# Optimization experiments

Hardware: AMD Instinct MI355X
Metric: run time of the kernel (lower is better)

The kernel has to match this reference:

```python
import jax, jax.numpy as jnp
import numpy as np

N = 50000      # nodes
E = 800000     # edges (before self-loops)
DIN, H1, H2, OUT = 128, 128, 64, 40
LN_EPS = 1e-5


def setup_inputs() -> dict:
    key = jax.random.key(0)
    ks = jax.random.split(key, 16)
    s = lambda d: 1.0 / np.sqrt(d)
    inp = {
        "x": jax.random.normal(ks[0], (N, DIN), jnp.float32),
        "edge_index": jax.random.randint(ks[1], (2, E), 0, N, dtype=jnp.int64),
        # GCNConv weights (applied as x @ W) and biases
        "W1": jax.random.normal(ks[2], (DIN, H1), jnp.float32) * s(DIN),
        "b1": jnp.zeros((H1,), jnp.float32),
        "W2": jax.random.normal(ks[3], (H1, H2), jnp.float32) * s(H1),
        "b2": jnp.zeros((H2,), jnp.float32),
        "W3": jax.random.normal(ks[4], (H2, H2), jnp.float32) * s(H2),
        "b3": jnp.zeros((H2,), jnp.float32),
        # LayerNorms
        "g1": jnp.ones((H1,), jnp.float32),
        "be1": jnp.zeros((H1,), jnp.float32),
        "g2": jnp.ones((H2,), jnp.float32),
        "be2": jnp.zeros((H2,), jnp.float32),
        # post_mp MLP head
        "Wp1": jax.random.normal(ks[5], (H2, H2), jnp.float32) * s(H2),
        "bp1": jnp.zeros((H2,), jnp.float32),
        "Wp2": jax.random.normal(ks[6], (H2, OUT), jnp.float32) * s(H2),
        "bp2": jnp.zeros((OUT,), jnp.float32),
    }
    return inp


def _layer_norm(x, g, b):
    mu = jnp.mean(x, axis=-1, keepdims=True)
    var = jnp.mean((x - mu) ** 2, axis=-1, keepdims=True)
    return (x - mu) * jax.lax.rsqrt(var + LN_EPS) * g + b


def _gcn(x, src, dst, norm, W, b):
    # PyG GCNConv: linear first, then normalized gather/scatter-add, bias last
    h = x @ W                                  # [N, H]
    msg = h[src] * norm[:, None]               # [E+N, H] gather
    out = jax.ops.segment_sum(msg, dst, num_segments=N)  # scatter-add
    return out + b


def reference(x, edge_index, W1, b1, W2, b2, W3, b3, g1, be1, g2, be2,
              Wp1, bp1, Wp2, bp2):
    loops = jnp.arange(N, dtype=edge_index.dtype)
    src = jnp.concatenate([edge_index[0], loops])  # add self-loops
    dst = jnp.concatenate([edge_index[1], loops])
    # symmetric normalization D^{-1/2} (A+I) D^{-1/2} (same graph all layers)
    deg = jax.ops.segment_sum(jnp.ones_like(src, dtype=x.dtype), dst,
                              num_segments=N)
    dinv = jnp.where(deg > 0, jax.lax.rsqrt(jnp.maximum(deg, 1.0)), 0.0)
    norm = dinv[src] * dinv[dst]

    h = _gcn(x, src, dst, norm, W1, b1)
    h = _layer_norm(jax.nn.relu(h), g1, be1)
    h = _gcn(h, src, dst, norm, W2, b2)
    h = _layer_norm(jax.nn.relu(h), g2, be2)
    emb = _gcn(h, src, dst, norm, W3, b3)      # emb = conv output, pre-ReLU
    h = jax.nn.relu(emb)
    h = (h @ Wp1 + bp1) @ Wp2 + bp2            # post_mp: two stacked Linears
    return emb, jax.nn.log_softmax(h, axis=1)
```

## Files before the change

kernel.cpp:

```cpp
#include <hip/hip_runtime.h>
#include <hip/hip_bf16.h>

#define DIN 128
#define HID1 128
#define HID2 64
#define OUTD 40

typedef __attribute__((ext_vector_type(8))) short bf16x8;
typedef __attribute__((ext_vector_type(4))) float f32x4;

__device__ __forceinline__ float bf2f(unsigned int u) {
    union { unsigned int i; float f; } c;
    c.i = u << 16;
    return c.f;
}
__device__ __forceinline__ unsigned short f2bf(float f) {
    union { float f; unsigned int i; } c; c.f = f;
    unsigned int r = c.i + 0x7FFFu + ((c.i >> 16) & 1u);
    return (unsigned short)(r >> 16);
}
__device__ __forceinline__ unsigned int packbf(float lo, float hi) {
    return (unsigned int)f2bf(lo) | ((unsigned int)f2bf(hi) << 16);
}

__global__ void detect_kernel(const unsigned short* __restrict__ xu,
                              const int* __restrict__ ei, int* __restrict__ flags) {
    __shared__ int sh[2];
    if (threadIdx.x < 2) sh[threadIdx.x] = 0;
    __syncthreads();
    int bad = 0;
    for (int i = threadIdx.x; i < 2048; i += 256) {
        float v = bf2f(xu[2 * i]);
        float a = fabsf(v);
        if (!(a <= 1e4f) || (v != 0.f && a < 1e-4f)) bad++;
    }
    int zodd = 0;
    for (int i = threadIdx.x; i < 1024; i += 256)
        if (ei[2 * i + 1] == 0) zodd++;
    atomicAdd(&sh[0], bad);
    atomicAdd(&sh[1], zodd);
    __syncthreads();
    if (threadIdx.x == 0) {
        flags[0] = (sh[0] > 512) ? 1 : 0;
        flags[1] = (sh[1] > 512) ? 1 : 0;
    }
}

__device__ __forceinline__ int get_src(const int* ei, int E, int e, int e64) {
    return e64 ? ei[2 * e] : ei[e];
}
__device__ __forceinline__ int get_dst(const int* ei, int E, int e, int e64) {
    return e64 ? ei[2 * (E + e)] : ei[E + e];
}


__global__ void init_cnt_kernel(int* __restrict__ cnt, int N) {
    int i = blockIdx.x * blockDim.x + threadIdx.x;
    if (i < N) cnt[i] = 0;
}

__global__ void pos_kernel(const int* __restrict__ ei, int* __restrict__ cnt,
                           int* __restrict__ pos, int E, int N,
                           const int* __restrict__ flags) {
    int e64 = flags[1];
    int base = (blockIdx.x * blockDim.x + threadIdx.x) * 4;
    #pragma unroll
    for (int u = 0; u < 4; ++u) {
        int e = base + u;
        if (e < E) {
            int d = get_dst(ei, E, e, e64);
            pos[e] = ((unsigned)d < (unsigned)N) ? atomicAdd(&cnt[d], 1) : -1;
        }
    }
}


__launch_bounds__(256)
__global__ void bsum_kernel(const int* __restrict__ cnt, int* __restrict__ bsum, int N) {
    __shared__ int sh[256];
    int t = threadIdx.x;
    int i = blockIdx.x * 256 + t;
    sh[t] = (i < N) ? cnt[i] : 0;
    __syncthreads();
    #pragma unroll
    for (int off = 128; off >= 1; off >>= 1) {
        if (t < off) sh[t] += sh[t + off];
        __syncthreads();
    }
    if (t == 0) bsum[blockIdx.x] = sh[0];
}

__launch_bounds__(256)
__global__ void bscan_kernel(const int* __restrict__ bsum, int* __restrict__ bbase,
                             int* __restrict__ indptr, int NB, int N) {
    __shared__ int part[256];
    int t = threadIdx.x;
    int CH = (NB + 255) / 256;
    int lo = t * CH, hi = lo + CH; if (hi > NB) hi = NB;
    int s = 0;
    for (int i = lo; i < hi; ++i) s += bsum[i];
    part[t] = s;
    __syncthreads();
    for (int off = 1; off < 256; off <<= 1) {
        int v = (t >= off) ? part[t - off] : 0;
        __syncthreads();
        part[t] += v;
        __syncthreads();
    }
    int run = (t > 0) ? part[t - 1] : 0;
    for (int i = lo; i < hi; ++i) { bbase[i] = run; run += bsum[i]; }
    if (t == 255) indptr[N] = part[255];
}

__launch_bounds__(256)
__global__ void emit_kernel(const int* __restrict__ cnt, const int* __restrict__ bbase,
                            int* __restrict__ indptr, float* __restrict__ dinv, int N) {
    __shared__ int sh[256];
    int t = threadIdx.x;
    int i = blockIdx.x * 256 + t;
    int c = (i < N) ? cnt[i] : 0;
    sh[t] = c;
    __syncthreads();
    for (int off = 1; off < 256; off <<= 1) {
        int v = (t >= off) ? sh[t - off] : 0;
        __syncthreads();
        sh[t] += v;
        __syncthreads();
    }
    if (i < N) {
        int excl = sh[t] - c + bbase[blockIdx.x];
        indptr[i] = excl;
        dinv[i] = 1.0f / sqrtf((float)(c + 1));
    }
}

__global__ void scatter_kernel(const int* __restrict__ ei, const int* __restrict__ indptr,
                               const int* __restrict__ pos, int* __restrict__ csr_src,
                               int E, int N, const int* __restrict__ flags) {
    int e64 = flags[1];
    int base = (blockIdx.x * blockDim.x + threadIdx.x) * 4;
    #pragma unroll
    for (int u = 0; u < 4; ++u) {
        int e = base + u;
        if (e < E) {
            int p = pos[e];
            if (p >= 0) {
                int d = get_dst(ei, E, e, e64);
                int s = get_src(ei, E, e, e64);
                if ((unsigned)s >= (unsigned)N) s = 0;
                csr_src[indptr[d] + p] = s;
            }
        }
    }
}


struct WCvt {
    const void* p[14];
    int sz[14];
    int off[14];
    int tobf[14];
    int cols[14];
};

__global__ void wcvt_kernel(WCvt w, unsigned short* __restrict__ wbf,
                            float* __restrict__ wf, const int* __restrict__ flags) {
    int xf32 = flags[0];
    int stride = gridDim.x * blockDim.x;
    int tid = blockIdx.x * blockDim.x + threadIdx.x;
    for (int a = 0; a < 14; ++a) {
        const float* pf = (const float*)w.p[a];
        const unsigned short* pb = (const unsigned short*)w.p[a];
        int n = w.sz[a], off = w.off[a], tobf = w.tobf[a];
        int cols = w.cols[a];
        int rows = tobf ? (n / cols) : 0;
        for (int i = tid; i < n; i += stride) {
            float v = xf32 ? pf[i] : bf2f(pb[i]);
            if (tobf) {
                int k = i / cols, m = i % cols;
                wbf[off + m * rows + k] = f2bf(v);
            } else {
                wf[off + i] = v;
            }
        }
    }
}

__global__ void xcvt_kernel(const float* __restrict__ xf, unsigned short* __restrict__ xbf,
                            int n, const int* __restrict__ flags) {
    if (!flags[0]) return;
    int stride = gridDim.x * blockDim.x;
    for (int i = blockIdx.x * blockDim.x + threadIdx.x; i < n; i += stride)
        xbf[i] = f2bf(xf[i]);
}


template<int K, int M>
__launch_bounds__(256)
__global__ void mm_mfma_kernel(const unsigned short* __restrict__ A0,
                               const unsigned short* __restrict__ A1,
                               const unsigned short* __restrict__ WT,
                               unsigned short* __restrict__ C, int N,
                               const int* __restrict__ flags, int useAlt) {
    __shared__ unsigned short Ws[M][K + 8];
    const unsigned short* A = (useAlt && flags[0]) ? A1 : A0;
    int tid = threadIdx.x;
    for (int idx = tid; idx < M * K / 8; idx += 256) {
        int r = idx / (K / 8), c8 = idx % (K / 8);
        *(uint4*)&Ws[r][c8 * 8] = *(const uint4*)&WT[r * K + c8 * 8];
    }
    __syncthreads();
    int w = tid >> 6, lane = tid & 63;
    int m = lane & 15, q = lane >> 4;
    int row_a = blockIdx.x * 64 + w * 16 + m;
    if (row_a >= N) row_a = N - 1;
    const unsigned short* arow = A + (size_t)row_a * K;
    f32x4 acc[M / 16];
    #pragma unroll
    for (int t = 0; t < M / 16; ++t) acc[t] = (f32x4){0.f, 0.f, 0.f, 0.f};
    #pragma unroll
    for (int ks = 0; ks < K / 32; ++ks) {
        int k0 = ks * 32 + q * 8;
        bf16x8 a = *(const bf16x8*)&arow[k0];
        #pragma unroll
        for (int t = 0; t < M / 16; ++t) {
            bf16x8 b = *(const bf16x8*)&Ws[t * 16 + m][k0];
            acc[t] = __builtin_amdgcn_mfma_f32_16x16x32_bf16(a, b, acc[t], 0, 0, 0);
        }
    }
    int rbase = blockIdx.x * 64 + w * 16 + q * 4;
    #pragma unroll
    for (int reg = 0; reg < 4; ++reg) {
        int row = rbase + reg;
        if (row < N) {
            #pragma unroll
            for (int t = 0; t < M / 16; ++t)
                C[(size_t)row * M + t * 16 + m] = f2bf(acc[t][reg]);
        }
    }
}


template<int VPL>
__device__ __forceinline__ void gacc(float* acc, const unsigned short* r, float n) {
    if constexpr (VPL == 8) {
        uint4 u = *(const uint4*)r;
        acc[0] += bf2f(u.x & 0xffffu) * n; acc[1] += bf2f(u.x >> 16) * n;
        acc[2] += bf2f(u.y & 0xffffu) * n; acc[3] += bf2f(u.y >> 16) * n;
        acc[4] += bf2f(u.z & 0xffffu) * n; acc[5] += bf2f(u.z >> 16) * n;
        acc[6] += bf2f(u.w & 0xffffu) * n; acc[7] += bf2f(u.w >> 16) * n;
    } else {
        uint2 u = *(const uint2*)r;
        acc[0] += bf2f(u.x & 0xffffu) * n; acc[1] += bf2f(u.x >> 16) * n;
        acc[2] += bf2f(u.y & 0xffffu) * n; acc[3] += bf2f(u.y >> 16) * n;
    }
}

template<int VPL>
__device__ __forceinline__ void gacc2(float* acc, const unsigned short* r0, float n0,
                                      const unsigned short* r1, float n1) {
    if constexpr (VPL == 8) {
        uint4 u0 = *(const uint4*)r0;
        uint4 u1 = *(const uint4*)r1;
        acc[0] += bf2f(u0.x & 0xffffu) * n0 + bf2f(u1.x & 0xffffu) * n1;
        acc[1] += bf2f(u0.x >> 16) * n0 + bf2f(u1.x >> 16) * n1;
        acc[2] += bf2f(u0.y & 0xffffu) * n0 + bf2f(u1.y & 0xffffu) * n1;
        acc[3] += bf2f(u0.y >> 16) * n0 + bf2f(u1.y >> 16) * n1;
        acc[4] += bf2f(u0.z & 0xffffu) * n0 + bf2f(u1.z & 0xffffu) * n1;
        acc[5] += bf2f(u0.z >> 16) * n0 + bf2f(u1.z >> 16) * n1;
        acc[6] += bf2f(u0.w & 0xffffu) * n0 + bf2f(u1.w & 0xffffu) * n1;
        acc[7] += bf2f(u0.w >> 16) * n0 + bf2f(u1.w >> 16) * n1;
    } else {
        uint2 u0 = *(const uint2*)r0;
        uint2 u1 = *(const uint2*)r1;
        acc[0] += bf2f(u0.x & 0xffffu) * n0 + bf2f(u1.x & 0xffffu) * n1;
        acc[1] += bf2f(u0.x >> 16) * n0 + bf2f(u1.x >> 16) * n1;
        acc[2] += bf2f(u0.y & 0xffffu) * n0 + bf2f(u1.y & 0xffffu) * n1;
        acc[3] += bf2f(u0.y >> 16) * n0 + bf2f(u1.y >> 16) * n1;
    }
}

template<int H, bool RELU_LN, bool EMB>
__launch_bounds__(256)
__global__ void agg_kernel(const unsigned short* __restrict__ h,
                           const int* __restrict__ indptr,
                           const int* __restrict__ csr_src,
                           const float* __restrict__ dinv,
                           const float* __restrict__ bias,
                           const float* __restrict__ gamma,
                           const float* __restrict__ beta,
                           unsigned short* __restrict__ out,
                           void* __restrict__ out_emb,
                           int N, const int* __restrict__ flags) {
    constexpr int VPL = H / 16;
    __shared__ int   lsrc[4][64];
    __shared__ float lnrm[4][64];
    int w = threadIdx.x >> 6;
    int lane = threadIdx.x & 63;
    int ql = lane >> 4;
    int g = lane & 15;
    int node = blockIdx.x * 4 + w;
    if (node >= N) return;
    float di = dinv[node];
    int c0 = g * VPL;
    float acc[VPL];
    #pragma unroll
    for (int v = 0; v < VPL; ++v) acc[v] = 0.f;
    gacc<VPL>(acc, h + (size_t)node * H + c0, (ql == 0) ? di * di : 0.f);
    int beg = indptr[node], end = indptr[node + 1];
    for (int base = beg; base < end; base += 64) {
        int m = end - base; if (m > 64) m = 64;
        if (lane < m) {
            int s = csr_src[base + lane];
            if ((unsigned)s >= (unsigned)N) s = 0;
            lsrc[w][lane] = s;
            lnrm[w][lane] = dinv[s] * di;
        }
        int j = ql;
        for (; j + 4 < m; j += 8) {
            int s0 = lsrc[w][j], s1 = lsrc[w][j + 4];
            float n0 = lnrm[w][j], n1 = lnrm[w][j + 4];
            gacc2<VPL>(acc, h + (size_t)s0 * H + c0, n0, h + (size_t)s1 * H + c0, n1);
        }
        if (j < m)
            gacc<VPL>(acc, h + (size_t)lsrc[w][j] * H + c0, lnrm[w][j]);
    }
    #pragma unroll
    for (int v = 0; v < VPL; ++v) acc[v] += __shfl_xor(acc[v], 16, 64);
    #pragma unroll
    for (int v = 0; v < VPL; ++v) acc[v] += __shfl_xor(acc[v], 32, 64);
    #pragma unroll
    for (int v = 0; v < VPL; ++v) acc[v] += bias[c0 + v];
    if constexpr (RELU_LN) {
        #pragma unroll
        for (int v = 0; v < VPL; ++v) acc[v] = fmaxf(acc[v], 0.f);
        float s = 0.f, sq = 0.f;
        #pragma unroll
        for (int v = 0; v < VPL; ++v) { s += acc[v]; sq += acc[v] * acc[v]; }
        #pragma unroll
        for (int off = 8; off >= 1; off >>= 1) {
            s += __shfl_xor(s, off, 64);
            sq += __shfl_xor(sq, off, 64);
        }
        float mu = s * (1.0f / H);
        float var = fmaxf(sq * (1.0f / H) - mu * mu, 0.f);
        float inv = 1.0f / sqrtf(var + 1e-5f);
        #pragma unroll
        for (int v = 0; v < VPL; ++v)
            acc[v] = (acc[v] - mu) * inv * gamma[c0 + v] + beta[c0 + v];
    }
    if (ql == 0) {
        unsigned short* orow = out + (size_t)node * H + c0;
        if constexpr (VPL == 8) {
            uint4 p;
            p.x = packbf(acc[0], acc[1]); p.y = packbf(acc[2], acc[3]);
            p.z = packbf(acc[4], acc[5]); p.w = packbf(acc[6], acc[7]);
            *(uint4*)orow = p;
        } else {
            uint2 p; p.x = packbf(acc[0], acc[1]); p.y = packbf(acc[2], acc[3]);
            *(uint2*)orow = p;
        }
        if constexpr (EMB) {
            if (flags[0]) {
                float* o = (float*)out_emb + (size_t)node * H + c0;
                #pragma unroll
                for (int v4 = 0; v4 < VPL / 4; ++v4)
                    *(float4*)(o + v4 * 4) = make_float4(acc[v4 * 4], acc[v4 * 4 + 1],
                                                         acc[v4 * 4 + 2], acc[v4 * 4 + 3]);
            } else {
                unsigned short* o = (unsigned short*)out_emb + (size_t)node * H + c0;
                #pragma unroll
                for (int v2 = 0; v2 < VPL / 2; ++v2)
                    ((unsigned int*)o)[v2] = packbf(acc[v2 * 2], acc[v2 * 2 + 1]);
            }
        }
    }
}


__launch_bounds__(256)
__global__ void head_kernel(const unsigned short* __restrict__ emb,
                            const float* __restrict__ Wp1,
                            const float* __restrict__ bp1,
                            const float* __restrict__ Wp2,
                            const float* __restrict__ bp2,
                            void* __restrict__ d_out, int N,
                            const int* __restrict__ flags) {
    __shared__ float Est[64][68];
    __shared__ float W1s[64][64];
    __shared__ float Tst[64][68];
    __shared__ float W2s[64][OUTD];
    __shared__ float b1s[64];
    __shared__ float b2s[OUTD];
    int tid = threadIdx.x;
    int row0 = blockIdx.x * 64;
    for (int i = tid; i < 64 * 64; i += 256) W1s[i >> 6][i & 63] = Wp1[i];
    for (int i = tid; i < 64 * OUTD; i += 256) W2s[i / OUTD][i % OUTD] = Wp2[i];
    if (tid < 64) b1s[tid] = bp1[tid];
    if (tid < OUTD) b2s[tid] = bp2[tid];
    for (int i = tid; i < 64 * 32; i += 256) {
        int r = i >> 5, kk = i & 31;
        int row = row0 + r;
        unsigned int u = (row < N) ? *(const unsigned int*)&emb[(size_t)row * 64 + kk * 2] : 0u;
        Est[kk * 2][r]     = fmaxf(bf2f(u & 0xffffu), 0.f);
        Est[kk * 2 + 1][r] = fmaxf(bf2f(u >> 16), 0.f);
    }
    __syncthreads();
    {
        int rg = tid >> 4, cg = tid & 15;
        int r = rg * 4, c = cg * 4;
        float acc[4][4];
        #pragma unroll
        for (int i = 0; i < 4; ++i)
            #pragma unroll
            for (int jj = 0; jj < 4; ++jj) acc[i][jj] = b1s[c + jj];
        #pragma unroll 4
        for (int k = 0; k < 64; ++k) {
            float4 a = *(const float4*)&Est[k][r];
            float4 wv = *(const float4*)&W1s[k][c];
            acc[0][0] += a.x * wv.x; acc[0][1] += a.x * wv.y; acc[0][2] += a.x * wv.z; acc[0][3] += a.x * wv.w;
            acc[1][0] += a.y * wv.x; acc[1][1] += a.y * wv.y; acc[1][2] += a.y * wv.z; acc[1][3] += a.y * wv.w;
            acc[2][0] += a.z * wv.x; acc[2][1] += a.z * wv.y; acc[2][2] += a.z * wv.z; acc[2][3] += a.z * wv.w;
            acc[3][0] += a.w * wv.x; acc[3][1] += a.w * wv.y; acc[3][2] += a.w * wv.z; acc[3][3] += a.w * wv.w;
        }
        #pragma unroll
        for (int i = 0; i < 4; ++i)
            #pragma unroll
            for (int jj = 0; jj < 4; ++jj) Tst[c + jj][r + i] = acc[i][jj];
    }
    __syncthreads();
    int row = tid >> 2, tc = tid & 3, o0 = tc * 10;
    int node = row0 + row;
    float u[10];
    #pragma unroll
    for (int o = 0; o < 10; ++o) u[o] = b2s[o0 + o];
    for (int c2 = 0; c2 < 64; ++c2) {
        float tv = Tst[c2][row];
        const float2* wp = (const float2*)&W2s[c2][o0];
        #pragma unroll
        for (int o2 = 0; o2 < 5; ++o2) {
            float2 wv = wp[o2];
            u[o2 * 2]     += tv * wv.x;
            u[o2 * 2 + 1] += tv * wv.y;
        }
    }
    float mx = u[0];
    #pragma unroll
    for (int o = 1; o < 10; ++o) mx = fmaxf(mx, u[o]);
    mx = fmaxf(mx, __shfl_xor(mx, 1, 64));
    mx = fmaxf(mx, __shfl_xor(mx, 2, 64));
    float sum = 0.f;
    #pragma unroll
    for (int o = 0; o < 10; ++o) sum += __expf(u[o] - mx);
    sum += __shfl_xor(sum, 1, 64);
    sum += __shfl_xor(sum, 2, 64);
    float lse = mx + __logf(sum);
    if (node < N) {
        if (flags[0]) {
            float* base = (float*)d_out + (size_t)N * HID2;
            float* op = base + (size_t)node * OUTD + o0;
            #pragma unroll
            for (int o = 0; o < 10; ++o) op[o] = u[o] - lse;
        } else {
            unsigned short* base = (unsigned short*)d_out + (size_t)N * HID2;
            unsigned int* op = (unsigned int*)(base + (size_t)node * OUTD + o0);
            #pragma unroll
            for (int o2 = 0; o2 < 5; ++o2)
                op[o2] = packbf(u[o2 * 2] - lse, u[o2 * 2 + 1] - lse);
        }
    }
}


extern "C" void kernel_launch(void* const* d_in, const int* in_sizes, int n_in,
                              void* d_out, int out_size, void* d_ws, size_t ws_size,
                              hipStream_t stream) {
    const unsigned short* xu = (const unsigned short*)d_in[0];
    const float*          xf = (const float*)d_in[0];
    const int*            ei = (const int*)d_in[1];

    const int N = in_sizes[0] / DIN;
    const int E = in_sizes[1] / 2;

    size_t off = 0;
    auto take = [&](size_t bytes) {
        size_t cur = off;
        off += (bytes + 255) & ~(size_t)255;
        return cur;
    };
    char* ws = (char*)d_ws;
    int*   flags   = (int*)  (ws + take(256));
    int*   cnt     = (int*)  (ws + take((size_t)N * 4));
    float* dinv    = (float*)(ws + take((size_t)N * 4));
    int*   indptr  = (int*)  (ws + take((size_t)(N + 1) * 4));
    int*   pos     = (int*)  (ws + take((size_t)E * 4));
    int*   csr_src = (int*)  (ws + take((size_t)E * 4));
    int*   bsum    = (int*)  (ws + take(((size_t)N / 256 + 2) * 4));
    int*   bbase   = (int*)  (ws + take(((size_t)N / 256 + 2) * 4));
    unsigned short* wbf = (unsigned short*)(ws + take(32768 * 2));
    float*          wf  = (float*)         (ws + take(8192 * 4));
    unsigned short* hbuf = (unsigned short*)(ws + take((size_t)N * DIN * 2));
    unsigned short* abuf = (unsigned short*)(ws + take((size_t)N * DIN * 2));
    (void)ws_size; (void)n_in; (void)out_size;

    const int TB = 256;
    dim3 blk(TB);
    const int NB = (N + 255) / 256;

    detect_kernel<<<dim3(1), blk, 0, stream>>>(xu, ei, flags);
    init_cnt_kernel<<<dim3((N + TB - 1) / TB), blk, 0, stream>>>(cnt, N);
    pos_kernel<<<dim3((E + 1023) / 1024), blk, 0, stream>>>(ei, cnt, pos, E, N, flags);
    bsum_kernel<<<dim3(NB), blk, 0, stream>>>(cnt, bsum, N);
    bscan_kernel<<<dim3(1), blk, 0, stream>>>(bsum, bbase, indptr, NB, N);
    emit_kernel<<<dim3(NB), blk, 0, stream>>>(cnt, bbase, indptr, dinv, N);
    scatter_kernel<<<dim3((E + 1023) / 1024), blk, 0, stream>>>(ei, indptr, pos, csr_src, E, N, flags);

    WCvt w;
    int bfoff = 0, foff = 0;
    int offs[14];
    const int wcols[14] = {HID1, 0, HID2, 0, HID2, 0, 0, 0, 0, 0, 0, 0, 0, 0};
    for (int a = 0; a < 14; ++a) {
        int idx = a + 2;
        w.p[a] = d_in[idx];
        w.sz[a] = in_sizes[idx];
        int tobf = (idx == 2 || idx == 4 || idx == 6) ? 1 : 0;
        w.tobf[a] = tobf;
        w.cols[a] = tobf ? wcols[a] : 1;
        if (tobf) { w.off[a] = bfoff; bfoff += in_sizes[idx]; }
        else      { w.off[a] = foff;  foff  += in_sizes[idx]; }
        offs[a] = w.off[a];
    }
    wcvt_kernel<<<dim3(64), blk, 0, stream>>>(w, wbf, wf, flags);
    xcvt_kernel<<<dim3(512), blk, 0, stream>>>(xf, abuf, N * DIN, flags);

    unsigned short* W1t = wbf + offs[0];
    unsigned short* W2t = wbf + offs[2];
    unsigned short* W3t = wbf + offs[4];
    float* b1f  = wf + offs[1];
    float* b2f  = wf + offs[3];
    float* b3f  = wf + offs[5];
    float* g1f  = wf + offs[6];
    float* be1f = wf + offs[7];
    float* g2f  = wf + offs[8];
    float* be2f = wf + offs[9];
    float* Wp1f = wf + offs[10];
    float* bp1f = wf + offs[11];
    float* Wp2f = wf + offs[12];
    float* bp2f = wf + offs[13];

    const int MMG = (N + 63) / 64;

    mm_mfma_kernel<DIN, HID1><<<dim3(MMG), blk, 0, stream>>>(xu, abuf, W1t, hbuf, N, flags, 1);
    agg_kernel<HID1, true, false><<<dim3((N + 3) / 4), blk, 0, stream>>>(
        hbuf, indptr, csr_src, dinv, b1f, g1f, be1f, abuf, nullptr, N, flags);

    mm_mfma_kernel<HID1, HID2><<<dim3(MMG), blk, 0, stream>>>(abuf, nullptr, W2t, hbuf, N, flags, 0);
    agg_kernel<HID2, true, false><<<dim3((N + 3) / 4), blk, 0, stream>>>(
        hbuf, indptr, csr_src, dinv, b2f, g2f, be2f, abuf, nullptr, N, flags);

    mm_mfma_kernel<HID2, HID2><<<dim3(MMG), blk, 0, stream>>>(abuf, nullptr, W3t, hbuf, N, flags, 0);
    agg_kernel<HID2, false, true><<<dim3((N + 3) / 4), blk, 0, stream>>>(
        hbuf, indptr, csr_src, dinv, b3f, nullptr, nullptr, abuf, d_out, N, flags);

    head_kernel<<<dim3((N + 63) / 64), blk, 0, stream>>>(
        abuf, Wp1f, bp1f, Wp2f, bp2f, d_out, N, flags);
}
```

Before: 331.9 us.

## Precompute per-edge norms into packed CSR, unroll gather by four, merge init kernels

The scatter step now stores each edge's source index together with its precomputed normalization (dinv[src]*dinv[dst]) as an int2 in CSR order. The three aggregation kernels then read that pair directly instead of doing a dependent dinv[s] lookup for every edge in every layer. The gather loop now issues four neighbor row loads per iteration instead of two, to expose more memory-level parallelism. The detect and count-init kernels are merged into one launch. In exchange the CSR array doubles in size and the unrolled loop raises register pressure.

```diff
diff --git a/kernel.cpp b/kernel.cpp
--- a/kernel.cpp
+++ b/kernel.cpp
@@ -23,26 +23,31 @@
     return (unsigned int)f2bf(lo) | ((unsigned int)f2bf(hi) << 16);
 }
 
-__global__ void detect_kernel(const unsigned short* __restrict__ xu,
-                              const int* __restrict__ ei, int* __restrict__ flags) {
-    __shared__ int sh[2];
-    if (threadIdx.x < 2) sh[threadIdx.x] = 0;
-    __syncthreads();
-    int bad = 0;
-    for (int i = threadIdx.x; i < 2048; i += 256) {
-        float v = bf2f(xu[2 * i]);
-        float a = fabsf(v);
-        if (!(a <= 1e4f) || (v != 0.f && a < 1e-4f)) bad++;
-    }
-    int zodd = 0;
-    for (int i = threadIdx.x; i < 1024; i += 256)
-        if (ei[2 * i + 1] == 0) zodd++;
-    atomicAdd(&sh[0], bad);
-    atomicAdd(&sh[1], zodd);
-    __syncthreads();
-    if (threadIdx.x == 0) {
-        flags[0] = (sh[0] > 512) ? 1 : 0;
-        flags[1] = (sh[1] > 512) ? 1 : 0;
+__global__ void pre_kernel(const unsigned short* __restrict__ xu,
+                           const int* __restrict__ ei, int* __restrict__ flags,
+                           int* __restrict__ cnt, int N) {
+    int i = blockIdx.x * blockDim.x + threadIdx.x;
+    if (i < N) cnt[i] = 0;
+    if (blockIdx.x == 0) {
+        __shared__ int sh[2];
+        if (threadIdx.x < 2) sh[threadIdx.x] = 0;
+        __syncthreads();
+        int bad = 0;
+        for (int k = threadIdx.x; k < 2048; k += 256) {
+            float v = bf2f(xu[2 * k]);
+            float a = fabsf(v);
+            if (!(a <= 1e4f) || (v != 0.f && a < 1e-4f)) bad++;
+        }
+        int zodd = 0;
+        for (int k = threadIdx.x; k < 1024; k += 256)
+            if (ei[2 * k + 1] == 0) zodd++;
+        atomicAdd(&sh[0], bad);
+        atomicAdd(&sh[1], zodd);
+        __syncthreads();
+        if (threadIdx.x == 0) {
+            flags[0] = (sh[0] > 512) ? 1 : 0;
+            flags[1] = (sh[1] > 512) ? 1 : 0;
+        }
     }
 }
 
@@ -51,12 +56,6 @@
 }
 __device__ __forceinline__ int get_dst(const int* ei, int E, int e, int e64) {
     return e64 ? ei[2 * (E + e)] : ei[E + e];
-}
-
-
-__global__ void init_cnt_kernel(int* __restrict__ cnt, int N) {
-    int i = blockIdx.x * blockDim.x + threadIdx.x;
-    if (i < N) cnt[i] = 0;
 }
 
 __global__ void pos_kernel(const int* __restrict__ ei, int* __restrict__ cnt,
@@ -135,7 +134,8 @@
 }
 
 __global__ void scatter_kernel(const int* __restrict__ ei, const int* __restrict__ indptr,
-                               const int* __restrict__ pos, int* __restrict__ csr_src,
+                               const int* __restrict__ pos, const float* __restrict__ dinv,
+                               int2* __restrict__ csr_sn,
                                int E, int N, const int* __restrict__ flags) {
     int e64 = flags[1];
     int base = (blockIdx.x * blockDim.x + threadIdx.x) * 4;
@@ -148,7 +148,8 @@
                 int d = get_dst(ei, E, e, e64);
                 int s = get_src(ei, E, e, e64);
                 if ((unsigned)s >= (unsigned)N) s = 0;
-                csr_src[indptr[d] + p] = s;
+                float nrm = dinv[s] * dinv[d];
+                csr_sn[indptr[d] + p] = make_int2(s, __float_as_int(nrm));
             }
         }
     }
@@ -242,7 +243,7 @@
 
 
 template<int VPL>
-__device__ __forceinline__ void gacc(float* acc, const unsigned short* r, float n) {
+__device__ __forceinline__ void gacc1(float* acc, const unsigned short* r, float n) {
     if constexpr (VPL == 8) {
         uint4 u = *(const uint4*)r;
         acc[0] += bf2f(u.x & 0xffffu) * n; acc[1] += bf2f(u.x >> 16) * n;
@@ -257,26 +258,45 @@
 }
 
 template<int VPL>
-__device__ __forceinline__ void gacc2(float* acc, const unsigned short* r0, float n0,
-                                      const unsigned short* r1, float n1) {
+__device__ __forceinline__ void gacc4(float* acc,
+                                      const unsigned short* r0, float n0,
+                                      const unsigned short* r1, float n1,
+                                      const unsigned short* r2, float n2,
+                                      const unsigned short* r3, float n3) {
     if constexpr (VPL == 8) {
         uint4 u0 = *(const uint4*)r0;
         uint4 u1 = *(const uint4*)r1;
-        acc[0] += bf2f(u0.x & 0xffffu) * n0 + bf2f(u1.x & 0xffffu) * n1;
-        acc[1] += bf2f(u0.x >> 16) * n0 + bf2f(u1.x >> 16) * n1;
-        acc[2] += bf2f(u0.y & 0xffffu) * n0 + bf2f(u1.y & 0xffffu) * n1;
-        acc[3] += bf2f(u0.y >> 16) * n0 + bf2f(u1.y >> 16) * n1;
-        acc[4] += bf2f(u0.z & 0xffffu) * n0 + bf2f(u1.z & 0xffffu) * n1;
-        acc[5] += bf2f(u0.z >> 16) * n0 + bf2f(u1.z >> 16) * n1;
-        acc[6] += bf2f(u0.w & 0xffffu) * n0 + bf2f(u1.w & 0xffffu) * n1;
-        acc[7] += bf2f(u0.w >> 16) * n0 + bf2f(u1.w >> 16) * n1;
+        uint4 u2 = *(const uint4*)r2;
+        uint4 u3 = *(const uint4*)r3;
+        acc[0] += bf2f(u0.x & 0xffffu) * n0 + bf2f(u1.x & 0xffffu) * n1
+                + bf2f(u2.x & 0xffffu) * n2 + bf2f(u3.x & 0xffffu) * n3;
+        acc[1] += bf2f(u0.x >> 16) * n0 + bf2f(u1.x >> 16) * n1
+                + bf2f(u2.x >> 16) * n2 + bf2f(u3.x >> 16) * n3;
+        acc[2] += bf2f(u0.y & 0xffffu) * n0 + bf2f(u1.y & 0xffffu) * n1
+                + bf2f(u2.y & 0xffffu) * n2 + bf2f(u3.y & 0xffffu) * n3;
+        acc[3] += bf2f(u0.y >> 16) * n0 + bf2f(u1.y >> 16) * n1
+                + bf2f(u2.y >> 16) * n2 + bf2f(u3.y >> 16) * n3;
+        acc[4] += bf2f(u0.z & 0xffffu) * n0 + bf2f(u1.z & 0xffffu) * n1
+                + bf2f(u2.z & 0xffffu) * n2 + bf2f(u3.z & 0xffffu) * n3;
+        acc[5] += bf2f(u0.z >> 16) * n0 + bf2f(u1.z >> 16) * n1
+                + bf2f(u2.z >> 16) * n2 + bf2f(u3.z >> 16) * n3;
+        acc[6] += bf2f(u0.w & 0xffffu) * n0 + bf2f(u1.w & 0xffffu) * n1
+                + bf2f(u2.w & 0xffffu) * n2 + bf2f(u3.w & 0xffffu) * n3;
+        acc[7] += bf2f(u0.w >> 16) * n0 + bf2f(u1.w >> 16) * n1
+                + bf2f(u2.w >> 16) * n2 + bf2f(u3.w >> 16) * n3;
     } else {
         uint2 u0 = *(const uint2*)r0;
         uint2 u1 = *(const uint2*)r1;
-        acc[0] += bf2f(u0.x & 0xffffu) * n0 + bf2f(u1.x & 0xffffu) * n1;
-        acc[1] += bf2f(u0.x >> 16) * n0 + bf2f(u1.x >> 16) * n1;
-        acc[2] += bf2f(u0.y & 0xffffu) * n0 + bf2f(u1.y & 0xffffu) * n1;
-        acc[3] += bf2f(u0.y >> 16) * n0 + bf2f(u1.y >> 16) * n1;
+        uint2 u2 = *(const uint2*)r2;
+        uint2 u3 = *(const uint2*)r3;
+        acc[0] += bf2f(u0.x & 0xffffu) * n0 + bf2f(u1.x & 0xffffu) * n1
+                + bf2f(u2.x & 0xffffu) * n2 + bf2f(u3.x & 0xffffu) * n3;
+        acc[1] += bf2f(u0.x >> 16) * n0 + bf2f(u1.x >> 16) * n1
+                + bf2f(u2.x >> 16) * n2 + bf2f(u3.x >> 16) * n3;
+        acc[2] += bf2f(u0.y & 0xffffu) * n0 + bf2f(u1.y & 0xffffu) * n1
+                + bf2f(u2.y & 0xffffu) * n2 + bf2f(u3.y & 0xffffu) * n3;
+        acc[3] += bf2f(u0.y >> 16) * n0 + bf2f(u1.y >> 16) * n1
+                + bf2f(u2.y >> 16) * n2 + bf2f(u3.y >> 16) * n3;
     }
 }
 
@@ -284,7 +304,7 @@
 __launch_bounds__(256)
 __global__ void agg_kernel(const unsigned short* __restrict__ h,
                            const int* __restrict__ indptr,
-                           const int* __restrict__ csr_src,
+                           const int2* __restrict__ csr_sn,
                            const float* __restrict__ dinv,
                            const float* __restrict__ bias,
                            const float* __restrict__ gamma,
@@ -293,8 +313,7 @@
                            void* __restrict__ out_emb,
                            int N, const int* __restrict__ flags) {
     constexpr int VPL = H / 16;
-    __shared__ int   lsrc[4][64];
-    __shared__ float lnrm[4][64];
+    __shared__ int2 lsn[4][64];
     int w = threadIdx.x >> 6;
     int lane = threadIdx.x & 63;
     int ql = lane >> 4;
@@ -306,24 +325,24 @@
     float acc[VPL];
     #pragma unroll
     for (int v = 0; v < VPL; ++v) acc[v] = 0.f;
-    gacc<VPL>(acc, h + (size_t)node * H + c0, (ql == 0) ? di * di : 0.f);
+    gacc1<VPL>(acc, h + (size_t)node * H + c0, (ql == 0) ? di * di : 0.f);
     int beg = indptr[node], end = indptr[node + 1];
     for (int base = beg; base < end; base += 64) {
         int m = end - base; if (m > 64) m = 64;
-        if (lane < m) {
-            int s = csr_src[base + lane];
-            if ((unsigned)s >= (unsigned)N) s = 0;
-            lsrc[w][lane] = s;
-            lnrm[w][lane] = dinv[s] * di;
-        }
+        if (lane < m) lsn[w][lane] = csr_sn[base + lane];
         int j = ql;
-        for (; j + 4 < m; j += 8) {
-            int s0 = lsrc[w][j], s1 = lsrc[w][j + 4];
-            float n0 = lnrm[w][j], n1 = lnrm[w][j + 4];
-            gacc2<VPL>(acc, h + (size_t)s0 * H + c0, n0, h + (size_t)s1 * H + c0, n1);
-        }
-        if (j < m)
-            gacc<VPL>(acc, h + (size_t)lsrc[w][j] * H + c0, lnrm[w][j]);
+        for (; j + 12 < m; j += 16) {
+            int2 e0 = lsn[w][j], e1 = lsn[w][j + 4], e2 = lsn[w][j + 8], e3 = lsn[w][j + 12];
+            gacc4<VPL>(acc,
+                       h + (size_t)e0.x * H + c0, __int_as_float(e0.y),
+                       h + (size_t)e1.x * H + c0, __int_as_float(e1.y),
+                       h + (size_t)e2.x * H + c0, __int_as_float(e2.y),
+                       h + (size_t)e3.x * H + c0, __int_as_float(e3.y));
+        }
+        for (; j < m; j += 4) {
+            int2 e = lsn[w][j];
+            gacc1<VPL>(acc, h + (size_t)e.x * H + c0, __int_as_float(e.y));
+        }
     }
     #pragma unroll
     for (int v = 0; v < VPL; ++v) acc[v] += __shfl_xor(acc[v], 16, 64);
@@ -494,7 +513,7 @@
     float* dinv    = (float*)(ws + take((size_t)N * 4));
     int*   indptr  = (int*)  (ws + take((size_t)(N + 1) * 4));
     int*   pos     = (int*)  (ws + take((size_t)E * 4));
-    int*   csr_src = (int*)  (ws + take((size_t)E * 4));
+    int2*  csr_sn  = (int2*) (ws + take((size_t)E * 8));
     int*   bsum    = (int*)  (ws + take(((size_t)N / 256 + 2) * 4));
     int*   bbase   = (int*)  (ws + take(((size_t)N / 256 + 2) * 4));
     unsigned short* wbf = (unsigned short*)(ws + take(32768 * 2));
@@ -507,13 +526,12 @@
     dim3 blk(TB);
     const int NB = (N + 255) / 256;
 
-    detect_kernel<<<dim3(1), blk, 0, stream>>>(xu, ei, flags);
-    init_cnt_kernel<<<dim3((N + TB - 1) / TB), blk, 0, stream>>>(cnt, N);
+    pre_kernel<<<dim3(NB), blk, 0, stream>>>(xu, ei, flags, cnt, N);
     pos_kernel<<<dim3((E + 1023) / 1024), blk, 0, stream>>>(ei, cnt, pos, E, N, flags);
     bsum_kernel<<<dim3(NB), blk, 0, stream>>>(cnt, bsum, N);
     bscan_kernel<<<dim3(1), blk, 0, stream>>>(bsum, bbase, indptr, NB, N);
     emit_kernel<<<dim3(NB), blk, 0, stream>>>(cnt, bbase, indptr, dinv, N);
-    scatter_kernel<<<dim3((E + 1023) / 1024), blk, 0, stream>>>(ei, indptr, pos, csr_src, E, N, flags);
+    scatter_kernel<<<dim3((E + 1023) / 1024), blk, 0, stream>>>(ei, indptr, pos, dinv, csr_sn, E, N, flags);
 
     WCvt w;
     int bfoff = 0, foff = 0;
@@ -552,15 +570,15 @@
 
     mm_mfma_kernel<DIN, HID1><<<dim3(MMG), blk, 0, stream>>>(xu, abuf, W1t, hbuf, N, flags, 1);
     agg_kernel<HID1, true, false><<<dim3((N + 3) / 4), blk, 0, stream>>>(
-        hbuf, indptr, csr_src, dinv, b1f, g1f, be1f, abuf, nullptr, N, flags);
+        hbuf, indptr, csr_sn, dinv, b1f, g1f, be1f, abuf, nullptr, N, flags);
 
     mm_mfma_kernel<HID1, HID2><<<dim3(MMG), blk, 0, stream>>>(abuf, nullptr, W2t, hbuf, N, flags, 0);
     agg_kernel<HID2, true, false><<<dim3((N + 3) / 4), blk, 0, stream>>>(
-        hbuf, indptr, csr_src, dinv, b2f, g2f, be2f, abuf, nullptr, N, flags);
+        hbuf, indptr, csr_sn, dinv, b2f, g2f, be2f, abuf, nullptr, N, flags);
 
     mm_mfma_kernel<HID2, HID2><<<dim3(MMG), blk, 0, stream>>>(abuf, nullptr, W3t, hbuf, N, flags, 0);
     agg_kernel<HID2, false, true><<<dim3((N + 3) / 4), blk, 0, stream>>>(
-        hbuf, indptr, csr_src, dinv, b3f, nullptr, nullptr, abuf, d_out, N, flags);
+        hbuf, indptr, csr_sn, dinv, b3f, nullptr, nullptr, abuf, d_out, N, flags);
 
     head_kernel<<<dim3((N + 63) / 64), blk, 0, stream>>>(
         abuf, Wp1f, bp1f, Wp2f, bp2f, d_out, N, flags);
```

New measurement: 338.6 us. 1.02x slower.
